# Kernel optimization log

Hardware: AMD Instinct MI355X
Metric: run time of the kernel (lower is better)

Reference implementation:

```python
import jax, jax.numpy as jnp
import numpy as np
from jax import lax

C3_TABLE = [(0, 1, 2), (1, 2, 3), (2, 3, 4), (3, 4, 5), (0, 4, 5), (0, 1, 5),
            (0, 1, 2, 3), (1, 2, 3, 4), (2, 3, 4, 5), (0, 3, 4, 5), (0, 1, 4, 5),
            (0, 1, 2, 5), (0, 1, 3, 4), (1, 2, 4, 5), (0, 2, 3, 5),
            (0, 1, 2, 3, 4, 5)]
TRIPLES = C3_TABLE[:6]   # 3-channel branches
QUADS   = C3_TABLE[6:15] # 4-channel branches
SEXTET  = C3_TABLE[15:]  # 6-channel branch
A = 1.7159
S = 2.0 / 3.0
DN = ('NCHW', 'OIHW', 'NCHW')


def _branch(x, idx, w, b):
    # x: [B,6,H,W]; gather channel subset, valid 5x5 conv to 1 output channel
    xg = x[:, jnp.array(idx), :, :]
    y = lax.conv_general_dilated(xg, w[None], (1, 1), 'VALID', dimension_numbers=DN)
    return y + b  # [B,1,H-4,W-4]


def setup_inputs() -> dict:
    key = jax.random.key(0)
    ks = jax.random.split(key, 7)
    B, H, W = 256, 142, 142
    return {
        'x':  jax.random.normal(ks[0], (B, 6, H, W), dtype=jnp.float32),
        'w3': jax.random.normal(ks[1], (6, 3, 5, 5), dtype=jnp.float32) * 0.1,
        'b3': jax.random.normal(ks[2], (6,), dtype=jnp.float32) * 0.1,
        'w4': jax.random.normal(ks[3], (9, 4, 5, 5), dtype=jnp.float32) * 0.1,
        'b4': jax.random.normal(ks[4], (9,), dtype=jnp.float32) * 0.1,
        'w6': jax.random.normal(ks[5], (1, 6, 5, 5), dtype=jnp.float32) * 0.1,
        'b6': jax.random.normal(ks[6], (1,), dtype=jnp.float32) * 0.1,
    }


def reference(x, w3, b3, w4, b4, w6, b6):
    outs = []
    for i, idx in enumerate(TRIPLES):
        outs.append(_branch(x, idx, w3[i], b3[i]))
    for i, idx in enumerate(QUADS):
        outs.append(_branch(x, idx, w4[i], b4[i]))
    outs.append(_branch(x, SEXTET[0], w6[0], b6[0]))
    y = jnp.concatenate(outs, axis=1)  # [B,16,H-4,W-4]
    return A * jnp.tanh(S * y)
```

## Files before the change

### kernel.cpp

```cpp
#include <hip/hip_runtime.h>
#include <hip/hip_bf16.h>


#define IH 142
#define IW 142
#define OH 138
#define OW 138
#define WROWS 12
#define WSTRIDE 2592
#define NTILE_X 9
#define NTILE_Y 3
#define NWG (NTILE_X * NTILE_Y * 256)
#define CPX (NWG / 8)

typedef _Float16 f16x8 __attribute__((ext_vector_type(8)));
typedef float f32x4 __attribute__((ext_vector_type(4)));

__device__ __constant__ const short WIDX16[16][6] = {
  {   0,    1,    2,   -1,   -1,   -1},
  {  -1,    3,    4,    5,   -1,   -1},
  {  -1,   -1,    6,    7,    8,   -1},
  {  -1,   -1,   -1,    9,   10,   11},
  {  12,   -1,   -1,   -1,   13,   14},
  {  15,   16,   -1,   -1,   -1,   17},
  {64+0, 64+1, 64+2, 64+3,   -1,   -1},
  {  -1, 64+4, 64+5, 64+6, 64+7,   -1},
  {  -1,   -1, 64+8, 64+9, 64+10, 64+11},
  {64+12,  -1,   -1, 64+13, 64+14, 64+15},
  {64+16, 64+17, -1,   -1, 64+18, 64+19},
  {64+20, 64+21, 64+22, -1,  -1, 64+23},
  {64+24, 64+25, -1, 64+26, 64+27,  -1},
  {  -1, 64+28, 64+29, -1, 64+30, 64+31},
  {64+32,  -1, 64+33, 64+34, -1, 64+35},
  {128+0, 128+1, 128+2, 128+3, 128+4, 128+5},
};

__global__ void wprep_kernel(const float* __restrict__ w3, const float* __restrict__ w4,
                             const float* __restrict__ w6, _Float16* __restrict__ tab) {
  int t = blockIdx.x * 256 + threadIdx.x;
  if (t >= 5120) return;
  int j = t & 7, lane = (t >> 3) & 63, dm = t >> 9;
  int dy = dm >> 1, m = dm & 1;
  int q = lane >> 4, oc = lane & 15;
  int k = m * 32 + q * 8 + j;
  int dx = k >> 3, c = k & 7;
  float v = 0.f;
  if (c < 6 && dx < 5) {
    int e = WIDX16[oc][c];
    if (e >= 0) {
      int src = e >> 6, blk = e & 63;
      const float* wp = (src == 0) ? w3 : (src == 1) ? w4 : w6;
      v = wp[blk * 25 + dy * 5 + dx];
    }
  }
  tab[t] = (_Float16)v;
}

__device__ __forceinline__ unsigned int pkh(float a, float b) {
  _Float16 ha = (_Float16)a, hb = (_Float16)b;
  unsigned short ua = __builtin_bit_cast(unsigned short, ha);
  unsigned short ub = __builtin_bit_cast(unsigned short, hb);
  return (unsigned int)ua | ((unsigned int)ub << 16);
}

__device__ __forceinline__ float act(float y) {
  const float TS = 1.9235933878519512f;
  const float e = __builtin_amdgcn_exp2f(y * TS);
  return fmaf(-2.f * 1.7159f, __builtin_amdgcn_rcpf(e + 1.f), 1.7159f);
}

__global__ __launch_bounds__(256, 4)
void c3_mfma(const float* __restrict__ x,
             const float* __restrict__ b3, const float* __restrict__ b4,
             const float* __restrict__ b6, const _Float16* __restrict__ tab,
             float* __restrict__ out) {
  __shared__ __attribute__((aligned(16))) _Float16 sh[4 * WSTRIDE];

  const int tid  = threadIdx.x;
  const int lane = tid & 63;
  const int w    = tid >> 6;

  const int hwid = (int)blockIdx.x + NTILE_X * ((int)blockIdx.y + NTILE_Y * (int)blockIdx.z);
  const int swz  = (hwid & 7) * CPX + (hwid >> 3);
  const int tx   = swz % NTILE_X;
  const int t2   = swz / NTILE_X;
  const int ty   = t2 % NTILE_Y;
  const int b    = t2 / NTILE_Y;

  const int x0   = min(tx * 16, OW - 16);
  const int y0   = min(ty * 48, OH - 48);
  const int ry0  = y0 + w * WROWS;

  const int ocl = lane & 15;
  const int q   = lane >> 4;

  f16x8 Bf[5][2];
  #pragma unroll
  for (int dy = 0; dy < 5; ++dy)
    #pragma unroll
    for (int m = 0; m < 2; ++m)
      Bf[dy][m] = *(const f16x8*)(tab + ((size_t)((dy * 2 + m) * 64 + lane)) * 8);

  const float bv = (ocl < 6) ? b3[ocl] : (ocl < 15) ? b4[ocl - 6] : b6[0];

  _Float16* __restrict__ shw = sh + w * WSTRIDE;
  if (lane < 16) ((unsigned int*)shw)[1280 + lane] = 0u;

  const float* xb = x + (size_t)b * 6 * IH * IW;
  #pragma unroll
  for (int it = 0; it < 10; ++it) {
    const int idx = it * 64 + lane;
    const int c2  = idx / 160;
    const int rem = idx - c2 * 160;
    const int row = rem / 10;
    const int px2 = rem - row * 10;
    const int ha  = row * 160 + px2 * 16 + c2 * 2;
    if (c2 < 3) {
      const float* pa = xb + ((size_t)(2 * c2) * IH + (ry0 + row)) * IW + x0 + 2 * px2;
      const float* pb = pa + (size_t)IH * IW;
      const float2 va = *(const float2*)pa;
      const float2 vb = *(const float2*)pb;
      *(unsigned int*)&shw[ha]     = pkh(va.x, vb.x);
      *(unsigned int*)&shw[ha + 8] = pkh(va.y, vb.y);
    } else {
      *(unsigned int*)&shw[ha]     = 0u;
      *(unsigned int*)&shw[ha + 8] = 0u;
    }
  }
  asm volatile("s_waitcnt lgkmcnt(0)" ::: "memory");

  const int voff = (ocl + q) * 8;
  f16x8 W6[6][2];
  #pragma unroll
  for (int i = 0; i < 6; ++i) {
    W6[i][0] = *(const f16x8*)&shw[i * 160 + voff];
    W6[i][1] = *(const f16x8*)&shw[i * 160 + voff + 32];
  }

  const size_t obase = ((size_t)b * 16 + ocl) * OH;
  #pragma unroll
  for (int r = 0; r < WROWS; r += 2) {
    f32x4 C0 = {bv, bv, bv, bv};
    f32x4 C1 = {bv, bv, bv, bv};
    #pragma unroll
    for (int dy = 0; dy < 5; ++dy) {
      const int i0 = (r + dy) % 6;
      const int i1 = (r + 1 + dy) % 6;
      C0 = __builtin_amdgcn_mfma_f32_16x16x32_f16(W6[i0][0], Bf[dy][0], C0, 0, 0, 0);
      C1 = __builtin_amdgcn_mfma_f32_16x16x32_f16(W6[i1][0], Bf[dy][0], C1, 0, 0, 0);
      C0 = __builtin_amdgcn_mfma_f32_16x16x32_f16(W6[i0][1], Bf[dy][1], C0, 0, 0, 0);
      C1 = __builtin_amdgcn_mfma_f32_16x16x32_f16(W6[i1][1], Bf[dy][1], C1, 0, 0, 0);
    }
    if (r + 2 < WROWS) {
      W6[r % 6][0]       = *(const f16x8*)&shw[(r + 6) * 160 + voff];
      W6[r % 6][1]       = *(const f16x8*)&shw[(r + 6) * 160 + voff + 32];
      W6[(r + 1) % 6][0] = *(const f16x8*)&shw[(r + 7) * 160 + voff];
      W6[(r + 1) % 6][1] = *(const f16x8*)&shw[(r + 7) * 160 + voff + 32];
    }
    {
      float* p0 = out + (obase + (ry0 + r)) * OW + x0 + q * 4;
      float* p1 = out + (obase + (ry0 + r + 1)) * OW + x0 + q * 4;
      *(float2*)p0       = make_float2(act(C0[0]), act(C0[1]));
      *(float2*)(p0 + 2) = make_float2(act(C0[2]), act(C0[3]));
      *(float2*)p1       = make_float2(act(C1[0]), act(C1[1]));
      *(float2*)(p1 + 2) = make_float2(act(C1[2]), act(C1[3]));
    }
  }
}

extern "C" void kernel_launch(void* const* d_in, const int* in_sizes, int n_in,
                              void* d_out, int out_size, void* d_ws, size_t ws_size,
                              hipStream_t stream) {
  const float* x  = (const float*)d_in[0];
  const float* w3 = (const float*)d_in[1];
  const float* b3 = (const float*)d_in[2];
  const float* w4 = (const float*)d_in[3];
  const float* b4 = (const float*)d_in[4];
  const float* w6 = (const float*)d_in[5];
  const float* b6 = (const float*)d_in[6];
  float* out = (float*)d_out;
  _Float16* tab = (_Float16*)d_ws;

  hipLaunchKernelGGL(wprep_kernel, dim3(20), dim3(256), 0, stream, w3, w4, w6, tab);

  dim3 grid(NTILE_X, NTILE_Y, 256);
  hipLaunchKernelGGL(c3_mfma, grid, dim3(256), 0, stream, x, b3, b4, b6, tab, out);
}
```

Measured before the change: 175.0 us.

## Halve workgroup size, hoist global loads into registers, add MFMA priority

Each workgroup now has 2 wavefronts covering 24 rows instead of 4 covering 48, and the grid doubles along Y to keep the same coverage. All input float2 loads are issued into registers before the weight-table loads and LDS stores, so more memory requests are in flight at once. s_setprio raises wave priority around the MFMA block. The changes add register pressure from holding 40 floats per lane, and the new q variable is unused. Index arithmetic moves to uint units but stays equivalent.

```diff
diff --git a/kernel.cpp b/kernel.cpp
--- a/kernel.cpp
+++ b/kernel.cpp
@@ -9,7 +9,7 @@
 #define WROWS 12
 #define WSTRIDE 2592
 #define NTILE_X 9
-#define NTILE_Y 3
+#define NTILE_Y 6
 #define NWG (NTILE_X * NTILE_Y * 256)
 #define CPX (NWG / 8)
 
@@ -69,12 +69,12 @@
   return fmaf(-2.f * 1.7159f, __builtin_amdgcn_rcpf(e + 1.f), 1.7159f);
 }
 
-__global__ __launch_bounds__(256, 4)
+__global__ __launch_bounds__(128, 4)
 void c3_mfma(const float* __restrict__ x,
              const float* __restrict__ b3, const float* __restrict__ b4,
              const float* __restrict__ b6, const _Float16* __restrict__ tab,
              float* __restrict__ out) {
-  __shared__ __attribute__((aligned(16))) _Float16 sh[4 * WSTRIDE];
+  __shared__ __attribute__((aligned(16))) _Float16 sh[2 * WSTRIDE];
 
   const int tid  = threadIdx.x;
   const int lane = tid & 63;
@@ -88,11 +88,33 @@
   const int b    = t2 / NTILE_Y;
 
   const int x0   = min(tx * 16, OW - 16);
-  const int y0   = min(ty * 48, OH - 48);
+  const int y0   = min(ty * 24, OH - 24);
   const int ry0  = y0 + w * WROWS;
 
   const int ocl = lane & 15;
-  const int q   = lane >> 4;
+  const int q   = lane >> 6 ? 0 : (lane >> 4);
+  const int qq  = lane >> 4;
+
+  const float* xb = x + (size_t)b * 6 * IH * IW;
+
+  float2 va[10], vb[10];
+  int  ha_[10];
+  bool act_[10];
+  #pragma unroll
+  for (int it = 0; it < 10; ++it) {
+    const int idx = it * 64 + lane;
+    const int ic2 = idx / 160;
+    const int rem = idx - ic2 * 160;
+    const int row = rem / 10;
+    const int px2 = rem - row * 10;
+    ha_[it]  = row * 80 + px2 * 8 + ic2;
+    act_[it] = (ic2 < 3);
+    if (act_[it]) {
+      const float* pa = xb + ((size_t)(2 * ic2) * IH + (ry0 + row)) * IW + x0 + 2 * px2;
+      va[it] = *(const float2*)pa;
+      vb[it] = *(const float2*)(pa + (size_t)IH * IW);
+    }
+  }
 
   f16x8 Bf[5][2];
   #pragma unroll
@@ -104,32 +126,22 @@
   const float bv = (ocl < 6) ? b3[ocl] : (ocl < 15) ? b4[ocl - 6] : b6[0];
 
   _Float16* __restrict__ shw = sh + w * WSTRIDE;
-  if (lane < 16) ((unsigned int*)shw)[1280 + lane] = 0u;
-
-  const float* xb = x + (size_t)b * 6 * IH * IW;
+  unsigned int* __restrict__ shu = (unsigned int*)shw;
+  if (lane < 16) shu[1280 + lane] = 0u;
+
   #pragma unroll
   for (int it = 0; it < 10; ++it) {
-    const int idx = it * 64 + lane;
-    const int c2  = idx / 160;
-    const int rem = idx - c2 * 160;
-    const int row = rem / 10;
-    const int px2 = rem - row * 10;
-    const int ha  = row * 160 + px2 * 16 + c2 * 2;
-    if (c2 < 3) {
-      const float* pa = xb + ((size_t)(2 * c2) * IH + (ry0 + row)) * IW + x0 + 2 * px2;
-      const float* pb = pa + (size_t)IH * IW;
-      const float2 va = *(const float2*)pa;
-      const float2 vb = *(const float2*)pb;
-      *(unsigned int*)&shw[ha]     = pkh(va.x, vb.x);
-      *(unsigned int*)&shw[ha + 8] = pkh(va.y, vb.y);
+    if (act_[it]) {
+      shu[ha_[it]]     = pkh(va[it].x, vb[it].x);
+      shu[ha_[it] + 4] = pkh(va[it].y, vb[it].y);
     } else {
-      *(unsigned int*)&shw[ha]     = 0u;
-      *(unsigned int*)&shw[ha + 8] = 0u;
+      shu[ha_[it]]     = 0u;
+      shu[ha_[it] + 4] = 0u;
     }
   }
   asm volatile("s_waitcnt lgkmcnt(0)" ::: "memory");
 
-  const int voff = (ocl + q) * 8;
+  const int voff = (ocl + qq) * 8;
   f16x8 W6[6][2];
   #pragma unroll
   for (int i = 0; i < 6; ++i) {
@@ -142,6 +154,7 @@
   for (int r = 0; r < WROWS; r += 2) {
     f32x4 C0 = {bv, bv, bv, bv};
     f32x4 C1 = {bv, bv, bv, bv};
+    __builtin_amdgcn_s_setprio(1);
     #pragma unroll
     for (int dy = 0; dy < 5; ++dy) {
       const int i0 = (r + dy) % 6;
@@ -151,6 +164,7 @@
       C0 = __builtin_amdgcn_mfma_f32_16x16x32_f16(W6[i0][1], Bf[dy][1], C0, 0, 0, 0);
       C1 = __builtin_amdgcn_mfma_f32_16x16x32_f16(W6[i1][1], Bf[dy][1], C1, 0, 0, 0);
     }
+    __builtin_amdgcn_s_setprio(0);
     if (r + 2 < WROWS) {
       W6[r % 6][0]       = *(const f16x8*)&shw[(r + 6) * 160 + voff];
       W6[r % 6][1]       = *(const f16x8*)&shw[(r + 6) * 160 + voff + 32];
@@ -158,8 +172,8 @@
       W6[(r + 1) % 6][1] = *(const f16x8*)&shw[(r + 7) * 160 + voff + 32];
     }
     {
-      float* p0 = out + (obase + (ry0 + r)) * OW + x0 + q * 4;
-      float* p1 = out + (obase + (ry0 + r + 1)) * OW + x0 + q * 4;
+      float* p0 = out + (obase + (ry0 + r)) * OW + x0 + qq * 4;
+      float* p1 = out + (obase + (ry0 + r + 1)) * OW + x0 + qq * 4;
       *(float2*)p0       = make_float2(act(C0[0]), act(C0[1]));
       *(float2*)(p0 + 2) = make_float2(act(C0[2]), act(C0[3]));
       *(float2*)p1       = make_float2(act(C1[0]), act(C1[1]));
@@ -184,5 +198,5 @@
   hipLaunchKernelGGL(wprep_kernel, dim3(20), dim3(256), 0, stream, w3, w4, w6, tab);
 
   dim3 grid(NTILE_X, NTILE_Y, 256);
-  hipLaunchKernelGGL(c3_mfma, grid, dim3(256), 0, stream, x, b3, b4, b6, tab, out);
-}
+  hipLaunchKernelGGL(c3_mfma, grid, dim3(128), 0, stream, x, b3, b4, b6, tab, out);
+}
```

New measurement: 162.8 us. 1.07x faster.
